# Performance work log

Measured on AMD Instinct MI355X. Metric: run time of the kernel, lower is better.

Reference implementation:

```python
import jax, jax.numpy as jnp
import numpy as np

D_MODEL = 1024
NUM_HEADS = 16
HEAD_DIM = D_MODEL // NUM_HEADS


def setup_inputs() -> dict:
    key = jax.random.key(0)
    ks = jax.random.split(key, 9)
    B, S = 4, 2048
    # xavier_uniform with gain=0.1 for square d_model x d_model weights
    limit = 0.1 * np.sqrt(6.0 / (D_MODEL + D_MODEL))
    def w(k):
        return jax.random.uniform(k, (D_MODEL, D_MODEL), jnp.float32, -limit, limit)
    return {
        "x": jax.random.normal(ks[0], (B, S, D_MODEL), jnp.float32),
        "wq": w(ks[1]), "bq": jnp.zeros((D_MODEL,), jnp.float32),
        "wk": w(ks[2]), "bk": jnp.zeros((D_MODEL,), jnp.float32),
        "wv": w(ks[3]), "bv": jnp.zeros((D_MODEL,), jnp.float32),
        "wo": w(ks[4]), "bo": jnp.zeros((D_MODEL,), jnp.float32),
    }


def reference(x, wq, bq, wk, bk, wv, bv, wo, bo):
    B, S, D = x.shape
    H, Hd = NUM_HEADS, HEAD_DIM
    scale = Hd ** -0.5
    # torch Linear: x @ W.T + b
    def proj(w, b):
        y = jnp.einsum('bsd,ed->bse', x, w) + b
        return y.reshape(B, S, H, Hd).transpose(0, 2, 1, 3)  # [B,H,S,Hd]
    q = proj(wq, bq)
    k = proj(wk, bk)
    v = proj(wv, bv)
    scores = jnp.einsum('bhqd,bhkd->bhqk', q, k) * scale  # [B,H,S,S]
    attn = jax.nn.softmax(scores, axis=-1)
    out = jnp.einsum('bhqk,bhkd->bhqd', attn, v)  # [B,H,S,Hd]
    out = out.transpose(0, 2, 1, 3).reshape(B, S, D)
    return jnp.einsum('bsd,ed->bse', out, wo) + bo
```

## Files before the change

### kernel.cpp

```cpp
#include <hip/hip_runtime.h>
#include <stdint.h>

#define SEQ 2048
#define NH 16
#define HD 64
#define DM 1024
#define MTOT 8192
#define BHCOUNT 64

typedef __attribute__((ext_vector_type(8))) short bf16x8;
typedef __attribute__((ext_vector_type(4))) float f32x4;
typedef __attribute__((ext_vector_type(16))) float f32x16;
typedef __attribute__((ext_vector_type(2))) float f32x2;

union U4 { unsigned u[4]; bf16x8 v; };

__device__ __forceinline__ unsigned short f2bf(float f) {
  union { float f; unsigned u; } v; v.f = f;
  return (unsigned short)((v.u + 0x7FFFu + ((v.u >> 16) & 1u)) >> 16);
}

#if __has_builtin(__builtin_amdgcn_cvt_pk_bf16_f32)
typedef __attribute__((ext_vector_type(2))) __bf16 bf16x2_t;
__device__ __forceinline__ unsigned pk_bf16(float a, float b) {
  bf16x2_t r = __builtin_amdgcn_cvt_pk_bf16_f32(a, b);
  union { bf16x2_t v; unsigned u; } c; c.v = r; return c.u;
}
#else
__device__ __forceinline__ unsigned pk_bf16(float a, float b) {
  return (unsigned)f2bf(a) | ((unsigned)f2bf(b) << 16);
}
#endif

__device__ __forceinline__ void gl_lds16(const void* g, void* l) {
  __builtin_amdgcn_global_load_lds((const __attribute__((address_space(1))) void*)g,
                                   (__attribute__((address_space(3))) void*)l, 16, 0, 0);
}

__device__ __forceinline__ f32x2 exp2_pk(f32x2 x) {
  f32x2 t = x * 0.05550411f + 0.24022651f;
  t = x * t + 0.69314718f;
  return x * t + 1.0f;
}

#if __has_builtin(__builtin_amdgcn_permlane32_swap)
__device__ __forceinline__ void pl32swap(unsigned& a, unsigned& b) {
  auto r = __builtin_amdgcn_permlane32_swap(a, b, false, false);
  a = r[0]; b = r[1];
}
#else
__device__ __forceinline__ void pl32swap(unsigned& a, unsigned& b) {
  asm("v_permlane32_swap_b32 %0, %1" : "+v"(a), "+v"(b));
}
#endif

__device__ __forceinline__ f32x16 fz16() {
  f32x16 v = {0.f, 0.f, 0.f, 0.f, 0.f, 0.f, 0.f, 0.f,
              0.f, 0.f, 0.f, 0.f, 0.f, 0.f, 0.f, 0.f};
  return v;
}

__global__ __launch_bounds__(256) void cvt_all_kernel(
    const float* __restrict__ x, const float* __restrict__ wq,
    const float* __restrict__ wk, const float* __restrict__ wv,
    const float* __restrict__ wo, unsigned short* __restrict__ xb,
    unsigned short* __restrict__ wqb, unsigned short* __restrict__ wkb,
    unsigned short* __restrict__ wvb, unsigned short* __restrict__ wob) {
  int blk = blockIdx.x;
  const float* src;
  unsigned short* dst;
  int off;
  if (blk < 8192)       { src = x;  dst = xb;  off = blk; }
  else if (blk < 9216)  { src = wq; dst = wqb; off = blk - 8192; }
  else if (blk < 10240) { src = wk; dst = wkb; off = blk - 9216; }
  else if (blk < 11264) { src = wv; dst = wvb; off = blk - 10240; }
  else                  { src = wo; dst = wob; off = blk - 11264; }
  int i = off * 256 + threadIdx.x;
  float4 f = ((const float4*)src)[i];
  uint2 o;
  o.x = pk_bf16(f.x, f.y);
  o.y = pk_bf16(f.z, f.w);
  ((uint2*)dst)[i] = o;
}

__device__ __forceinline__ void gemm_mainloop(const unsigned short* __restrict__ Am,
                                              const unsigned short* __restrict__ Bm,
                                              int rowBase, int colBase,
                                              unsigned short* smem, f32x4 (&acc)[4][2]) {
  unsigned short* sA = smem;
  unsigned short* sB = smem + 16384;
  const int tid = threadIdx.x;
  const int lane = tid & 63;
  const int wave = tid >> 6;
  const int quad = lane >> 4;
  const int l16 = lane & 15;
  const int wm = wave >> 2, wn = wave & 3;

#pragma unroll
  for (int i = 0; i < 4; i++)
#pragma unroll
    for (int j = 0; j < 2; j++) acc[i][j] = (f32x4){0.f, 0.f, 0.f, 0.f};

  const unsigned short* ast[2];
  const unsigned short* bst[2];
  int ldso[2];
#pragma unroll
  for (int l = 0; l < 2; l++) {
    int c = l * 512 + tid;
    int row = c >> 3;
    int ccg = (c & 7) ^ (row & 7);
    ast[l] = Am + (size_t)(rowBase + row) * DM + ccg * 8;
    bst[l] = Bm + (size_t)(colBase + row) * DM + ccg * 8;
    ldso[l] = c * 8;
  }

  auto stage = [&](unsigned short* Ad, unsigned short* Bd) {
#pragma unroll
    for (int l = 0; l < 2; l++) {
      gl_lds16(ast[l], Ad + ldso[l]);
      gl_lds16(bst[l], Bd + ldso[l]);
      ast[l] += 64;
      bst[l] += 64;
    }
  };

  auto compute = [&](const unsigned short* Ab, const unsigned short* Bb) {
#pragma unroll
    for (int kk = 0; kk < 2; kk++) {
      bf16x8 af[4], bfr[2];
#pragma unroll
      for (int i = 0; i < 4; i++)
        af[i] = *(const bf16x8*)(Ab + (wm * 64 + i * 16 + l16) * 64 +
                                 ((((kk << 2) + quad) ^ (l16 & 7)) << 3));
#pragma unroll
      for (int j = 0; j < 2; j++)
        bfr[j] = *(const bf16x8*)(Bb + (wn * 32 + j * 16 + l16) * 64 +
                                  ((((kk << 2) + quad) ^ (l16 & 7)) << 3));
#pragma unroll
      for (int i = 0; i < 4; i++)
#pragma unroll
        for (int j = 0; j < 2; j++)
          acc[i][j] = __builtin_amdgcn_mfma_f32_16x16x32_bf16(af[i], bfr[j], acc[i][j], 0, 0, 0);
    }
  };

  stage(sA, sB);

  for (int it2 = 0; it2 < 8; ++it2) {
    stage(sA + 8192, sB + 8192);
    asm volatile("s_waitcnt vmcnt(4)" ::: "memory");
    __builtin_amdgcn_s_barrier();
    compute(sA, sB);
    __builtin_amdgcn_s_barrier();
    if (it2 < 7) {
      stage(sA, sB);
      asm volatile("s_waitcnt vmcnt(4)" ::: "memory");
    } else {
      asm volatile("s_waitcnt vmcnt(0)" ::: "memory");
    }
    __builtin_amdgcn_s_barrier();
    compute(sA + 8192, sB + 8192);
    __builtin_amdgcn_s_barrier();
  }
}

#define QSCALE 0.18033688011112042f
#define TPAD 131

__global__ __launch_bounds__(512) void qkv_gemm_kernel(
    const unsigned short* __restrict__ xb,
    const unsigned short* __restrict__ wqb, const unsigned short* __restrict__ wkb,
    const unsigned short* __restrict__ wvb,
    const float* __restrict__ bq, const float* __restrict__ bk, const float* __restrict__ bv,
    unsigned short* __restrict__ qo, unsigned short* __restrict__ ko,
    unsigned short* __restrict__ vtb) {
  __shared__ unsigned short smem[32768];
  const int z = blockIdx.z;
  const unsigned short* wb = (z == 0) ? wqb : ((z == 1) ? wkb : wvb);
  const float* bias = (z == 0) ? bq : ((z == 1) ? bk : bv);

  const int rowBase = blockIdx.x * 128;
  const int colBase = blockIdx.y * 128;
  f32x4 acc[4][2];
  gemm_mainloop(xb, wb, rowBase, colBase, smem, acc);

  const int tid = threadIdx.x;
  const int lane = tid & 63;
  const int wave = tid >> 6;
  const int quad = lane >> 4;
  const int l16 = lane & 15;
  const int wm = wave >> 2, wn = wave & 3;

  if (z < 2) {
    unsigned short* out = (z == 0) ? qo : ko;
    const float oscale = (z == 0) ? QSCALE : 1.0f;
#pragma unroll
    for (int j = 0; j < 2; j++) {
      int col = colBase + wn * 32 + j * 16 + l16;
      float bb = bias[col];
      int h = col >> 6, hd = col & 63;
#pragma unroll
      for (int i = 0; i < 4; i++) {
#pragma unroll
        for (int r = 0; r < 4; r++) {
          int row = rowBase + wm * 64 + i * 16 + quad * 4 + r;
          int b = row >> 11, s = row & (SEQ - 1);
          out[(((size_t)b * NH + h) * SEQ + s) * HD + hd] = f2bf((acc[i][j][r] + bb) * oscale);
        }
      }
    }
  } else {
#pragma unroll
    for (int j = 0; j < 2; j++) {
      int e_local = wn * 32 + j * 16 + l16;
      float bb = bias[colBase + e_local];
#pragma unroll
      for (int i = 0; i < 4; i++) {
#pragma unroll
        for (int r = 0; r < 4; r++) {
          int s_local = wm * 64 + i * 16 + quad * 4 + r;
          smem[s_local * TPAD + e_local] = f2bf(acc[i][j][r] + bb);
        }
      }
    }
    __syncthreads();
    const int b = rowBase >> 11;
    const int sBase = rowBase & (SEQ - 1);
#pragma unroll
    for (int l = 0; l < 4; l++) {
      int chunk = l * 512 + tid;
      int e = chunk >> 4;
      int s8 = (chunk & 15) * 8;
      ushort4 v0, v1;
      v0.x = smem[(s8 + 0) * TPAD + e]; v0.y = smem[(s8 + 1) * TPAD + e];
      v0.z = smem[(s8 + 2) * TPAD + e]; v0.w = smem[(s8 + 3) * TPAD + e];
      v1.x = smem[(s8 + 4) * TPAD + e]; v1.y = smem[(s8 + 5) * TPAD + e];
      v1.z = smem[(s8 + 6) * TPAD + e]; v1.w = smem[(s8 + 7) * TPAD + e];
      int head = (colBase >> 6) + (e >> 6);
      int hd = e & 63;
      size_t base = (((size_t)(b * NH + head)) * HD + hd) * SEQ + sBase + s8;
      *(ushort4*)(vtb + base) = v0;
      *(ushort4*)(vtb + base + 4) = v1;
    }
  }
}

__global__ __launch_bounds__(256, 2) void flash_kernel(const unsigned short* __restrict__ q,
                                                       const unsigned short* __restrict__ k,
                                                       const unsigned short* __restrict__ vt,
                                                       unsigned short* __restrict__ ctx) {
  const int lid = blockIdx.x;
  const int xcd = lid & 7, idx = lid >> 3;
  const int bh = xcd * 8 + (idx >> 3);
  const int b = bh >> 4, h = bh & 15;
  const int q0 = (idx & 7) * 256;
  const int tid = threadIdx.x;
  const int wave = tid >> 6, lane = tid & 63;
  const int n = lane & 31, hi = lane >> 5;

  __shared__ __align__(16) unsigned short lds[24576];

  const unsigned short* qbh = q + (size_t)bh * SEQ * HD;
  const unsigned short* kbh = k + (size_t)bh * SEQ * HD;
  const unsigned short* vbh = vt + (size_t)bh * HD * SEQ;

  bf16x8 qf[2][4];
#pragma unroll
  for (int qs = 0; qs < 2; qs++)
#pragma unroll
    for (int hb = 0; hb < 4; hb++)
      qf[qs][hb] = *(const bf16x8*)(qbh + (size_t)(q0 + wave * 64 + qs * 32 + n) * HD +
                                    hb * 16 + hi * 8);

  f32x16 Ov[2][2];
#pragma unroll
  for (int qs = 0; qs < 2; qs++) { Ov[qs][0] = fz16(); Ov[qs][1] = fz16(); }
  f32x2 l2[2] = {{0.f, 0.f}, {0.f, 0.f}};

  int offB[2][4];
#pragma unroll
  for (int a = 0; a < 2; a++)
#pragma unroll
    for (int c = 0; c < 4; c++)
      offB[a][c] = (a * 32 + n) * 128 + ((((c << 1) | hi) ^ (n & 7)) << 4);

  const unsigned short* kst[2];
  const unsigned short* vst[2];
  int ldso[2];
#pragma unroll
  for (int l = 0; l < 2; l++) {
    int c = l * 256 + tid;
    int row = c >> 3;
    int ccg = (c & 7) ^ (row & 7);
    kst[l] = kbh + (size_t)row * HD + ccg * 8;
    vst[l] = vbh + (size_t)row * SEQ + ccg * 8;
    ldso[l] = c * 8;
  }

  auto stage_into = [&](unsigned short* Kd) {
#pragma unroll
    for (int l = 0; l < 2; l++) {
      gl_lds16(kst[l], Kd + ldso[l]);
      gl_lds16(vst[l], Kd + 4096 + ldso[l]);
      kst[l] += 64 * HD;
      vst[l] += 64;
    }
  };

  auto softmax_pk = [&](const f32x16& s, f32x2& lac, U4& pa, U4& pb) {
    unsigned u0, u1, u2, u3, u4, u5, u6, u7;
    f32x2 p;
    p = exp2_pk((f32x2){s[0], s[1]});   lac += p; u0 = pk_bf16(p[0], p[1]);
    p = exp2_pk((f32x2){s[2], s[3]});   lac += p; u1 = pk_bf16(p[0], p[1]);
    p = exp2_pk((f32x2){s[4], s[5]});   lac += p; u2 = pk_bf16(p[0], p[1]);
    p = exp2_pk((f32x2){s[6], s[7]});   lac += p; u3 = pk_bf16(p[0], p[1]);
    p = exp2_pk((f32x2){s[8], s[9]});   lac += p; u4 = pk_bf16(p[0], p[1]);
    p = exp2_pk((f32x2){s[10], s[11]}); lac += p; u5 = pk_bf16(p[0], p[1]);
    p = exp2_pk((f32x2){s[12], s[13]}); lac += p; u6 = pk_bf16(p[0], p[1]);
    p = exp2_pk((f32x2){s[14], s[15]}); lac += p; u7 = pk_bf16(p[0], p[1]);
    pl32swap(u0, u2);
    pl32swap(u1, u3);
    pl32swap(u4, u6);
    pl32swap(u5, u7);
    pa.u[0] = u0; pa.u[1] = u1; pa.u[2] = u2; pa.u[3] = u3;
    pb.u[0] = u4; pb.u[1] = u5; pb.u[2] = u6; pb.u[3] = u7;
  };

  auto compute = [&](const unsigned short* Kbase) {
    const char* Kc = (const char*)Kbase;
    const char* Vc = (const char*)(Kbase + 4096);
#pragma unroll
    for (int kb = 0; kb < 2; kb++) {
      bf16x8 kf0 = *(const bf16x8*)(Kc + offB[kb][0]);
      bf16x8 kf1 = *(const bf16x8*)(Kc + offB[kb][1]);
      bf16x8 kf2 = *(const bf16x8*)(Kc + offB[kb][2]);
      bf16x8 kf3 = *(const bf16x8*)(Kc + offB[kb][3]);
      __builtin_amdgcn_s_setprio(1);
      f32x16 sa = __builtin_amdgcn_mfma_f32_32x32x16_bf16(kf0, qf[0][0], fz16(), 0, 0, 0);
      f32x16 sb = __builtin_amdgcn_mfma_f32_32x32x16_bf16(kf0, qf[1][0], fz16(), 0, 0, 0);
      sa = __builtin_amdgcn_mfma_f32_32x32x16_bf16(kf1, qf[0][1], sa, 0, 0, 0);
      sb = __builtin_amdgcn_mfma_f32_32x32x16_bf16(kf1, qf[1][1], sb, 0, 0, 0);
      sa = __builtin_amdgcn_mfma_f32_32x32x16_bf16(kf2, qf[0][2], sa, 0, 0, 0);
      sb = __builtin_amdgcn_mfma_f32_32x32x16_bf16(kf2, qf[1][2], sb, 0, 0, 0);
      sa = __builtin_amdgcn_mfma_f32_32x32x16_bf16(kf3, qf[0][3], sa, 0, 0, 0);
      sb = __builtin_amdgcn_mfma_f32_32x32x16_bf16(kf3, qf[1][3], sb, 0, 0, 0);
      __builtin_amdgcn_s_setprio(0);

      U4 paA, pbA, paB, pbB;
      softmax_pk(sa, l2[0], paA, pbA);
      softmax_pk(sb, l2[1], paB, pbB);

      __builtin_amdgcn_s_setprio(1);
#pragma unroll
      for (int jo = 0; jo < 2; jo++) {
        bf16x8 v0 = *(const bf16x8*)(Vc + offB[jo][2 * kb + 0]);
        Ov[0][jo] = __builtin_amdgcn_mfma_f32_32x32x16_bf16(paA.v, v0, Ov[0][jo], 0, 0, 0);
        Ov[1][jo] = __builtin_amdgcn_mfma_f32_32x32x16_bf16(paB.v, v0, Ov[1][jo], 0, 0, 0);
        bf16x8 v1 = *(const bf16x8*)(Vc + offB[jo][2 * kb + 1]);
        Ov[0][jo] = __builtin_amdgcn_mfma_f32_32x32x16_bf16(pbA.v, v1, Ov[0][jo], 0, 0, 0);
        Ov[1][jo] = __builtin_amdgcn_mfma_f32_32x32x16_bf16(pbB.v, v1, Ov[1][jo], 0, 0, 0);
      }
      __builtin_amdgcn_s_setprio(0);
    }
  };

  unsigned short* rb0 = lds;
  unsigned short* rb1 = lds + 8192;
  unsigned short* rb2 = lds + 16384;

  stage_into(rb0);
  stage_into(rb1);
  asm volatile("s_waitcnt vmcnt(4)" ::: "memory");
  __builtin_amdgcn_s_barrier();

#pragma unroll 1
  for (int t = 0; t < 32; ++t) {
    if (t < 30) stage_into(rb2);
    compute(rb0);
    if (t < 31) {
      if (t < 30)
        asm volatile("s_waitcnt vmcnt(4)" ::: "memory");
      else
        asm volatile("s_waitcnt vmcnt(0)" ::: "memory");
      __builtin_amdgcn_s_barrier();
    }
    unsigned short* tmp = rb0; rb0 = rb1; rb1 = rb2; rb2 = tmp;
  }

#pragma unroll
  for (int qs = 0; qs < 2; qs++) {
    float lt = l2[qs][0] + l2[qs][1];
    lt += __shfl_xor(lt, 32);
    float invq = 1.0f / lt;
#pragma unroll
    for (int r = 0; r < 16; r++) {
      int qrow = (r & 3) + 8 * (r >> 2) + 4 * hi;
      float inv = __shfl(invq, qrow);
      int s = q0 + wave * 64 + qs * 32 + qrow;
      size_t base = (((size_t)b * SEQ + s) * NH + h) * HD;
      ctx[base + n] = f2bf(Ov[qs][0][r] * inv);
      ctx[base + 32 + n] = f2bf(Ov[qs][1][r] * inv);
    }
  }
}

__global__ __launch_bounds__(512) void out_gemm_kernel(const unsigned short* __restrict__ ab,
                                                       const unsigned short* __restrict__ wb,
                                                       const float* __restrict__ bias,
                                                       float* __restrict__ out) {
  __shared__ unsigned short smem[32768];
  const int rowBase = blockIdx.x * 128;
  const int colBase = blockIdx.y * 128;
  f32x4 acc[4][2];
  gemm_mainloop(ab, wb, rowBase, colBase, smem, acc);

  const int lane = threadIdx.x & 63;
  const int wave = threadIdx.x >> 6;
  const int quad = lane >> 4;
  const int l16 = lane & 15;
  const int wm = wave >> 2, wn = wave & 3;
#pragma unroll
  for (int j = 0; j < 2; j++) {
    int col = colBase + wn * 32 + j * 16 + l16;
    float bb = bias[col];
#pragma unroll
    for (int i = 0; i < 4; i++) {
#pragma unroll
      for (int r = 0; r < 4; r++) {
        int row = rowBase + wm * 64 + i * 16 + quad * 4 + r;
        out[(size_t)row * DM + col] = acc[i][j][r] + bb;
      }
    }
  }
}

extern "C" void kernel_launch(void* const* d_in, const int* in_sizes, int n_in,
                              void* d_out, int out_size, void* d_ws, size_t ws_size,
                              hipStream_t stream) {
  const float* x  = (const float*)d_in[0];
  const float* wq = (const float*)d_in[1];
  const float* bq = (const float*)d_in[2];
  const float* wk = (const float*)d_in[3];
  const float* bk = (const float*)d_in[4];
  const float* wv = (const float*)d_in[5];
  const float* bv = (const float*)d_in[6];
  const float* wo = (const float*)d_in[7];
  const float* bo = (const float*)d_in[8];
  float* out = (float*)d_out;

  unsigned short* ws = (unsigned short*)d_ws;
  unsigned short* xb   = ws;
  unsigned short* wqb  = xb + (size_t)MTOT * DM;
  unsigned short* wkb  = wqb + (size_t)DM * DM;
  unsigned short* wvb  = wkb + (size_t)DM * DM;
  unsigned short* wob  = wvb + (size_t)DM * DM;
  unsigned short* qb   = wob + (size_t)DM * DM;
  unsigned short* kb   = qb + (size_t)MTOT * DM;
  unsigned short* vtb  = kb + (size_t)MTOT * DM;
  unsigned short* ctx  = xb;

  cvt_all_kernel<<<12288, 256, 0, stream>>>(x, wq, wk, wv, wo, xb, wqb, wkb, wvb, wob);

  qkv_gemm_kernel<<<dim3(64, 8, 3), 512, 0, stream>>>(xb, wqb, wkb, wvb, bq, bk, bv,
                                                      qb, kb, vtb);
  flash_kernel<<<512, 256, 0, stream>>>(qb, kb, vtb, ctx);
  out_gemm_kernel<<<dim3(64, 8), 512, 0, stream>>>(ctx, wob, bo, out);
}
```

Before: 264.1 us.

## Software-pipeline QK/softmax of next tile with PV of current tile

Splits the per-tile attention step into a QK+softmax stage and a PV stage, then interleaves the PV of tile t with the QK/softmax of tile t+1. LDS grows from three to four staging slots so that a tile's V data stays resident until its delayed PV runs, and the loop is unrolled by two with ping-pong P registers. The aim is to hide the softmax exp/pack latency behind independent MFMA work. In exchange it raises register pressure (two sets of P fragments) and LDS use, which could lower occupancy at two blocks per CU.

Result: slower. 330.9 us (+25.3%).

```diff
diff --git a/kernel.cpp b/kernel.cpp
--- a/kernel.cpp
+++ b/kernel.cpp
@@ -258,7 +258,7 @@
   const int wave = tid >> 6, lane = tid & 63;
   const int n = lane & 31, hi = lane >> 5;
 
-  __shared__ __align__(16) unsigned short lds[24576];
+  __shared__ __align__(16) unsigned short lds[32768];
 
   const unsigned short* qbh = q + (size_t)bh * SEQ * HD;
   const unsigned short* kbh = k + (size_t)bh * SEQ * HD;
@@ -326,9 +326,8 @@
     pb.u[0] = u4; pb.u[1] = u5; pb.u[2] = u6; pb.u[3] = u7;
   };
 
-  auto compute = [&](const unsigned short* Kbase) {
+  auto qksm = [&](const unsigned short* Kbase, U4 (&P)[8]) {
     const char* Kc = (const char*)Kbase;
-    const char* Vc = (const char*)(Kbase + 4096);
 #pragma unroll
     for (int kb = 0; kb < 2; kb++) {
       bf16x8 kf0 = *(const bf16x8*)(Kc + offB[kb][0]);
@@ -345,47 +344,66 @@
       sa = __builtin_amdgcn_mfma_f32_32x32x16_bf16(kf3, qf[0][3], sa, 0, 0, 0);
       sb = __builtin_amdgcn_mfma_f32_32x32x16_bf16(kf3, qf[1][3], sb, 0, 0, 0);
       __builtin_amdgcn_s_setprio(0);
-
-      U4 paA, pbA, paB, pbB;
-      softmax_pk(sa, l2[0], paA, pbA);
-      softmax_pk(sb, l2[1], paB, pbB);
-
-      __builtin_amdgcn_s_setprio(1);
+      softmax_pk(sa, l2[0], P[kb * 4 + 0], P[kb * 4 + 1]);
+      softmax_pk(sb, l2[1], P[kb * 4 + 2], P[kb * 4 + 3]);
+    }
+  };
+
+  auto pv = [&](const unsigned short* slotBase, U4 (&P)[8]) {
+    const char* Vc = (const char*)(slotBase + 4096);
+    __builtin_amdgcn_s_setprio(1);
+#pragma unroll
+    for (int kb = 0; kb < 2; kb++) {
 #pragma unroll
       for (int jo = 0; jo < 2; jo++) {
         bf16x8 v0 = *(const bf16x8*)(Vc + offB[jo][2 * kb + 0]);
-        Ov[0][jo] = __builtin_amdgcn_mfma_f32_32x32x16_bf16(paA.v, v0, Ov[0][jo], 0, 0, 0);
-        Ov[1][jo] = __builtin_amdgcn_mfma_f32_32x32x16_bf16(paB.v, v0, Ov[1][jo], 0, 0, 0);
+        Ov[0][jo] = __builtin_amdgcn_mfma_f32_32x32x16_bf16(P[kb * 4 + 0].v, v0, Ov[0][jo], 0, 0, 0);
+        Ov[1][jo] = __builtin_amdgcn_mfma_f32_32x32x16_bf16(P[kb * 4 + 2].v, v0, Ov[1][jo], 0, 0, 0);
         bf16x8 v1 = *(const bf16x8*)(Vc + offB[jo][2 * kb + 1]);
-        Ov[0][jo] = __builtin_amdgcn_mfma_f32_32x32x16_bf16(pbA.v, v1, Ov[0][jo], 0, 0, 0);
-        Ov[1][jo] = __builtin_amdgcn_mfma_f32_32x32x16_bf16(pbB.v, v1, Ov[1][jo], 0, 0, 0);
+        Ov[0][jo] = __builtin_amdgcn_mfma_f32_32x32x16_bf16(P[kb * 4 + 1].v, v1, Ov[0][jo], 0, 0, 0);
+        Ov[1][jo] = __builtin_amdgcn_mfma_f32_32x32x16_bf16(P[kb * 4 + 3].v, v1, Ov[1][jo], 0, 0, 0);
       }
-      __builtin_amdgcn_s_setprio(0);
-    }
-  };
-
-  unsigned short* rb0 = lds;
-  unsigned short* rb1 = lds + 8192;
-  unsigned short* rb2 = lds + 16384;
-
-  stage_into(rb0);
-  stage_into(rb1);
+    }
+    __builtin_amdgcn_s_setprio(0);
+  };
+
+  unsigned short* s0 = lds;
+  unsigned short* s1 = lds + 8192;
+  unsigned short* s2 = lds + 16384;
+  unsigned short* s3 = lds + 24576;
+
+  U4 PA[8], PB[8];
+
+  stage_into(s0);
+  stage_into(s1);
   asm volatile("s_waitcnt vmcnt(4)" ::: "memory");
   __builtin_amdgcn_s_barrier();
+  stage_into(s2);
+  qksm(s0, PA);
+  asm volatile("s_waitcnt vmcnt(4)" ::: "memory");
+  __builtin_amdgcn_s_barrier();
 
 #pragma unroll 1
-  for (int t = 0; t < 32; ++t) {
-    if (t < 30) stage_into(rb2);
-    compute(rb0);
-    if (t < 31) {
-      if (t < 30)
-        asm volatile("s_waitcnt vmcnt(4)" ::: "memory");
-      else
-        asm volatile("s_waitcnt vmcnt(0)" ::: "memory");
-      __builtin_amdgcn_s_barrier();
-    }
-    unsigned short* tmp = rb0; rb0 = rb1; rb1 = rb2; rb2 = tmp;
-  }
+  for (int i = 0; i < 15; ++i) {
+    stage_into(s3);
+    pv(s0, PA);
+    qksm(s1, PB);
+    asm volatile("s_waitcnt vmcnt(4)" ::: "memory");
+    __builtin_amdgcn_s_barrier();
+    if (i < 14) stage_into(s0);
+    pv(s1, PB);
+    qksm(s2, PA);
+    if (i < 14)
+      asm volatile("s_waitcnt vmcnt(4)" ::: "memory");
+    else
+      asm volatile("s_waitcnt vmcnt(0)" ::: "memory");
+    __builtin_amdgcn_s_barrier();
+    unsigned short* t0p = s0; s0 = s2; s2 = t0p;
+    unsigned short* t1p = s1; s1 = s3; s3 = t1p;
+  }
+  pv(s0, PA);
+  qksm(s1, PB);
+  pv(s1, PB);
 
 #pragma unroll
   for (int qs = 0; qs < 2; qs++) {
```
